# Kernel optimization log

Hardware: AMD Instinct MI355X
Metric: run time of the kernel (lower is better)

## Reference

```python
import jax, jax.numpy as jnp
import numpy as np
import math

B, C, IMG, P = 32, 3, 224, 16
E, DEPTH, H, MLP = 768, 12, 12, 3072
NP = (IMG // P) ** 2          # 196 patches
S = NP + 1                    # 197 tokens with cls
NCLS = 10
HD = E // H                   # 64 head dim
EPS = 1e-5


def setup_inputs() -> dict:
    key = jax.random.key(0)
    ks = iter(jax.random.split(key, 64))
    n = lambda shape, s=0.02: (jax.random.normal(next(ks), shape, jnp.float32) * s)
    inp = {
        "x": jax.random.normal(next(ks), (B, C, IMG, IMG), jnp.float32),
        "conv_w": n((E, C, P, P)),
        "conv_b": jnp.zeros((E,), jnp.float32),
        "cls_token": n((1, 1, E)),
        "pos_embed": n((1, S, E)),
        # stacked per-layer params, leading dim DEPTH; linear weights stored [in, out]
        "ln1_w": jnp.ones((DEPTH, E), jnp.float32),
        "ln1_b": jnp.zeros((DEPTH, E), jnp.float32),
        "qkv_w": n((DEPTH, E, 3 * E)),
        "qkv_b": jnp.zeros((DEPTH, 3 * E), jnp.float32),
        "proj_w": n((DEPTH, E, E)),
        "proj_b": jnp.zeros((DEPTH, E), jnp.float32),
        "ln2_w": jnp.ones((DEPTH, E), jnp.float32),
        "ln2_b": jnp.zeros((DEPTH, E), jnp.float32),
        "mlp_w1": n((DEPTH, E, MLP)),
        "mlp_b1": jnp.zeros((DEPTH, MLP), jnp.float32),
        "mlp_w2": n((DEPTH, MLP, E)),
        "mlp_b2": jnp.zeros((DEPTH, E), jnp.float32),
        "lnf_w": jnp.ones((E,), jnp.float32),
        "lnf_b": jnp.zeros((E,), jnp.float32),
        "head_w": n((E, NCLS)),
        "head_b": jnp.zeros((NCLS,), jnp.float32),
    }
    return inp


def layernorm(x, w, b):
    mu = jnp.mean(x, axis=-1, keepdims=True)
    var = jnp.mean(jnp.square(x - mu), axis=-1, keepdims=True)
    return (x - mu) * jax.lax.rsqrt(var + EPS) * w + b


def reference(x, conv_w, conv_b, cls_token, pos_embed,
              ln1_w, ln1_b, qkv_w, qkv_b, proj_w, proj_b,
              ln2_w, ln2_b, mlp_w1, mlp_b1, mlp_w2, mlp_b2,
              lnf_w, lnf_b, head_w, head_b):
    # --- patch embedding: stride-P, kernel-P conv == patchify + matmul ---
    g = IMG // P  # 14
    patches = x.reshape(B, C, g, P, g, P).transpose(0, 2, 4, 1, 3, 5).reshape(B, NP, C * P * P)
    wp = conv_w.reshape(E, C * P * P)
    tok = jnp.einsum('bpd,ed->bpe', patches, wp) + conv_b  # [B, NP, E]

    # cls token + positional embedding (dropout = identity at eval)
    h = jnp.concatenate([jnp.broadcast_to(cls_token, (B, 1, E)), tok], axis=1) + pos_embed

    scale = math.sqrt(HD)
    for i in range(DEPTH):
        # --- attention ---
        y = layernorm(h, ln1_w[i], ln1_b[i])
        qkv = (y @ qkv_w[i] + qkv_b[i]).reshape(B, S, 3, H, HD)
        q, k, v = qkv[:, :, 0], qkv[:, :, 1], qkv[:, :, 2]  # [B, S, H, HD]
        attn = jnp.einsum('bqhd,bkhd->bhqk', q, k) / scale
        attn = jax.nn.softmax(attn, axis=-1)
        o = jnp.einsum('bhqk,bkhd->bqhd', attn, v).reshape(B, S, E)
        h = h + (o @ proj_w[i] + proj_b[i])
        # --- MLP ---
        y = layernorm(h, ln2_w[i], ln2_b[i])
        y = jax.nn.gelu(y @ mlp_w1[i] + mlp_b1[i], approximate=False)
        h = h + (y @ mlp_w2[i] + mlp_b2[i])

    h = layernorm(h, lnf_w, lnf_b)
    return h[:, 0] @ head_w + head_b  # [B, NCLS]
```

## Files before the change

### kernel.cpp

```cpp
#include <hip/hip_runtime.h>


typedef __attribute__((ext_vector_type(8))) short short8;
typedef __attribute__((ext_vector_type(8))) unsigned short ushort8;
typedef __attribute__((ext_vector_type(4))) float f32x4;
typedef unsigned short u16;

#define DEV __device__ __forceinline__

DEV u16 f2bf(float f) {
  unsigned int u = __builtin_bit_cast(unsigned int, f);
  u += 0x7fffu + ((u >> 16) & 1u);
  return (u16)(u >> 16);
}
DEV float wred_sum(float v) {
  for (int o = 32; o; o >>= 1) v += __shfl_xor(v, o, 64);
  return v;
}
DEV void glds16(const void* gp, void* lp) {
  __builtin_amdgcn_global_load_lds(
      (const __attribute__((address_space(1))) void*)gp,
      (__attribute__((address_space(3))) void*)lp, 16, 0, 0);
}
DEV int xcd_swz(int flat, int nwg) {
  int q = nwg >> 3, r = nwg & 7;
  int x = flat & 7, o = flat >> 3;
  return (x < r ? x * (q + 1) : r * (q + 1) + (x - r) * q) + o;
}

__global__ __launch_bounds__(256) void cvt4_k(const float* __restrict__ s,
                                              u16* __restrict__ d, long n4) {
  long i = (long)blockIdx.x * 256 + threadIdx.x;
  if (i >= n4) return;
  float4 v = ((const float4*)s)[i];
  ushort4 o;
  o.x = f2bf(v.x); o.y = f2bf(v.y); o.z = f2bf(v.z); o.w = f2bf(v.w);
  ((ushort4*)d)[i] = o;
}

__global__ __launch_bounds__(256) void tpose_k(const float* __restrict__ s,
                                               u16* __restrict__ d, int K,
                                               int N) {
  __shared__ float t[32][33];
  const int bx = blockIdx.x;
  const int by = blockIdx.y;
  const size_t base = (size_t)blockIdx.z * K * N;
  const int c = threadIdx.x & 31, r0 = threadIdx.x >> 5;
#pragma unroll
  for (int i = 0; i < 4; ++i) {
    int r = r0 + i * 8;
    t[r][c] = s[base + (size_t)(by * 32 + r) * N + bx * 32 + c];
  }
  __syncthreads();
#pragma unroll
  for (int i = 0; i < 4; ++i) {
    int r = r0 + i * 8;
    d[base + (size_t)(bx * 32 + r) * K + by * 32 + c] = f2bf(t[c][r]);
  }
}

__global__ __launch_bounds__(256) void patch_k(const float* __restrict__ x,
                                               u16* __restrict__ pt) {
  int i = blockIdx.x * 256 + threadIdx.x;
  int d = i % 768;
  int bp = i / 768;
  int p = bp % 196, b = bp / 196;
  int c = d >> 8, pd = d & 255;
  int py = pd >> 4, px = pd & 15;
  int gy = p / 14, gx = p - gy * 14;
  size_t src = ((size_t)(b * 3 + c) * 224 + gy * 16 + py) * 224 + gx * 16 + px;
  pt[i] = f2bf(x[src]);
}

__global__ __launch_bounds__(256) void clspos_k(const float* __restrict__ cls,
                                                const float* __restrict__ pos,
                                                float* __restrict__ h) {
  int i = blockIdx.x * 256 + threadIdx.x;
  int b = i / 768, e = i - b * 768;
  h[(size_t)b * 197 * 768 + e] = cls[e] + pos[e];
}

template <int EPI, int BM>
__global__ __launch_bounds__(256) void gemmP(
    const u16* __restrict__ A, int lda, const u16* __restrict__ Bt, int ldb,
    const float* __restrict__ bias, u16* __restrict__ outb, int ldo,
    float* __restrict__ outf, const float* __restrict__ pos, int M, int N,
    int K) {
  constexpr int MI = BM / 32;
  __shared__ __align__(16) u16 Ak[2][BM * 32];
  __shared__ __align__(16) u16 Bk[2][128 * 32];
  const int tid = threadIdx.x;
  const int lane = tid & 63, wid = tid >> 6;
  const int wm = wid >> 1, wn = wid & 1;
  const int lg = lane >> 4, lr = lane & 15;
  const int nwg = gridDim.x * gridDim.y;
  const int wg = xcd_swz(blockIdx.y * gridDim.x + blockIdx.x, nwg);
  const int tn = wg % gridDim.x, tm = wg / gridDim.x;

  const int sr = lane >> 2;
  const int sc4 = (((lane & 3) ^ ((lane >> 3) & 3)) << 3);
  const u16* aSrc = A + (size_t)(tm * BM + wid * (BM / 4) + sr) * lda + sc4;
  const u16* bSrc = Bt + (size_t)(tn * 128 + wid * 32 + sr) * ldb + sc4;
  const size_t aRow16 = (size_t)16 * lda, bRow16 = (size_t)16 * ldb;

  auto stage = [&](int buf, int kt) {
    const u16* ak = aSrc + kt * 32;
    const u16* bk = bSrc + kt * 32;
    u16* ad = &Ak[buf][wid * (BM / 4) * 32];
    u16* bd = &Bk[buf][wid * 1024];
    glds16(ak, ad);
    if constexpr (BM == 128) glds16(ak + aRow16, ad + 512);
    glds16(bk, bd);
    glds16(bk + bRow16, bd + 512);
  };

  const int rp = (lg ^ ((lr >> 1) & 3)) << 3;
  f32x4 acc[MI][4] = {};
  auto compute = [&](int buf) {
    short8 af[MI], bfr[4];
#pragma unroll
    for (int i = 0; i < MI; ++i)
      af[i] =
          *(const short8*)(&Ak[buf][(wm * (BM / 2) + i * 16 + lr) * 32 + rp]);
#pragma unroll
    for (int i = 0; i < 4; ++i)
      bfr[i] = *(const short8*)(&Bk[buf][(wn * 64 + i * 16 + lr) * 32 + rp]);
#pragma unroll
    for (int mi = 0; mi < MI; ++mi)
#pragma unroll
      for (int ni = 0; ni < 4; ++ni)
        acc[mi][ni] = __builtin_amdgcn_mfma_f32_16x16x32_bf16(
            af[mi], bfr[ni], acc[mi][ni], 0, 0, 0);
  };

  const int nk = K >> 5;
  int cur = 0;
  stage(0, 0);
  __syncthreads();
  for (int kt = 0; kt < nk - 1; ++kt) {
    stage(cur ^ 1, kt + 1);
    compute(cur);
    __syncthreads();
    cur ^= 1;
  }
  compute(cur);

#pragma unroll
  for (int mi = 0; mi < MI; ++mi)
#pragma unroll
    for (int ni = 0; ni < 4; ++ni)
#pragma unroll
      for (int r = 0; r < 4; ++r) {
        int grow = tm * BM + wm * (BM / 2) + mi * 16 + lg * 4 + r;
        int gcol = tn * 128 + wn * 64 + ni * 16 + lr;
        if (grow < M) {
          float v = acc[mi][ni][r] + bias[gcol];
          if constexpr (EPI == 0) {
            outb[(size_t)grow * ldo + gcol] = f2bf(v);
          } else if constexpr (EPI == 1) {
            float u = __expf(-1.5957691216f * (v + 0.044715f * v * v * v));
            outb[(size_t)grow * ldo + gcol] = f2bf(v / (1.f + u));
          } else if constexpr (EPI == 2) {
            outf[(size_t)grow * ldo + gcol] += v;
          } else {
            int b = grow / 196, p = grow - b * 196;
            outf[(size_t)(grow + b + 1) * 768 + gcol] =
                v + pos[(size_t)(p + 1) * 768 + gcol];
          }
        }
      }
}

__global__ __launch_bounds__(64) void qksm_k(const u16* __restrict__ qkv,
                                             u16* __restrict__ P) {
  const int bh = blockIdx.x;
  const int qt = blockIdx.y;
  const int lane = threadIdx.x;
  const int lg = lane >> 4, lr = lane & 15;
  const int b = bh / 12, hh = bh - b * 12;
  const u16* base = qkv + (size_t)b * 197 * 2304 + hh * 64;
  int qrow = qt * 16 + lr;
  if (qrow > 196) qrow = 196;
  const u16* qp = base + (size_t)qrow * 2304 + lg * 8;
  short8 a0 = *(const short8*)(qp);
  short8 a1 = *(const short8*)(qp + 32);
  f32x4 c[13];
  const bool kval[2] = {true, (12 * 16 + lr) <= 196};
#pragma unroll
  for (int kt = 0; kt < 13; ++kt) {
    int krow = kt * 16 + lr;
    if (krow > 196) krow = 196;
    const u16* kp = base + 768 + (size_t)krow * 2304 + lg * 8;
    short8 b0 = *(const short8*)(kp);
    short8 b1 = *(const short8*)(kp + 32);
    f32x4 t = {0.f, 0.f, 0.f, 0.f};
    t = __builtin_amdgcn_mfma_f32_16x16x32_bf16(a0, b0, t, 0, 0, 0);
    c[kt] = __builtin_amdgcn_mfma_f32_16x16x32_bf16(a1, b1, t, 0, 0, 0);
  }
  float mr[4], sr_[4];
#pragma unroll
  for (int r = 0; r < 4; ++r) {
    float mm = -3.4e38f;
#pragma unroll
    for (int kt = 0; kt < 13; ++kt)
      if (kval[kt == 12]) mm = fmaxf(mm, c[kt][r] * 0.125f);
#pragma unroll
    for (int o = 1; o < 16; o <<= 1) mm = fmaxf(mm, __shfl_xor(mm, o, 64));
    mr[r] = mm;
  }
#pragma unroll
  for (int r = 0; r < 4; ++r) {
    float s = 0.f;
#pragma unroll
    for (int kt = 0; kt < 13; ++kt) {
      float e = kval[kt == 12] ? __expf(c[kt][r] * 0.125f - mr[r]) : 0.f;
      c[kt][r] = e;
      s += e;
    }
#pragma unroll
    for (int o = 1; o < 16; o <<= 1) s += __shfl_xor(s, o, 64);
    sr_[r] = 1.0f / s;
  }
  u16* pb = P + (size_t)bh * 197 * 224;
#pragma unroll
  for (int r = 0; r < 4; ++r) {
    int q = qt * 16 + lg * 4 + r;
    if (q < 197) {
#pragma unroll
      for (int kt = 0; kt < 13; ++kt)
        pb[(size_t)q * 224 + kt * 16 + lr] = f2bf(c[kt][r] * sr_[r]);
      pb[(size_t)q * 224 + 208 + lr] = 0;
    }
  }
}

__global__ __launch_bounds__(256) void pv_k(const u16* __restrict__ qkv,
                                            const u16* __restrict__ P,
                                            u16* __restrict__ o) {
  const int bh = blockIdx.x;
  const int b = bh / 12, hh = bh - b * 12;
  const int tid = threadIdx.x;
  const int lane = tid & 63, ct = tid >> 6;
  const int lg = lane >> 4, lr = lane & 15;
  const u16* vbase =
      qkv + (size_t)b * 197 * 2304 + 1536 + hh * 64 + ct * 16 + lr;
  short8 vf[7];
#pragma unroll
  for (int ks = 0; ks < 7; ++ks) {
    ushort8 t;
#pragma unroll
    for (int j = 0; j < 8; ++j) {
      int kk = ks * 32 + lg * 8 + j;
      if (kk > 196) kk = 196;
      t[j] = vbase[(size_t)kk * 2304];
    }
    vf[ks] = __builtin_bit_cast(short8, t);
  }
  const u16* pbase = P + (size_t)bh * 197 * 224;
  u16* ob = o + (size_t)b * 197 * 768 + hh * 64 + ct * 16;
  for (int qt = 0; qt < 13; ++qt) {
    int q = qt * 16 + lr;
    if (q > 196) q = 196;
    const u16* pp = pbase + (size_t)q * 224 + lg * 8;
    f32x4 acc = {0.f, 0.f, 0.f, 0.f};
#pragma unroll
    for (int ks = 0; ks < 7; ++ks) {
      short8 af = *(const short8*)(pp + ks * 32);
      acc = __builtin_amdgcn_mfma_f32_16x16x32_bf16(af, vf[ks], acc, 0, 0, 0);
    }
#pragma unroll
    for (int r = 0; r < 4; ++r) {
      int qq = qt * 16 + lg * 4 + r;
      if (qq < 197) ob[(size_t)qq * 768 + lr] = f2bf(acc[r]);
    }
  }
}

__global__ __launch_bounds__(256) void ln_k(const float* __restrict__ x,
                                            const float* __restrict__ w,
                                            const float* __restrict__ bb,
                                            u16* __restrict__ y) {
  const int r = blockIdx.x, tid = threadIdx.x;
  const float* xr = x + (size_t)r * 768;
  float v0 = xr[tid], v1 = xr[tid + 256], v2 = xr[tid + 512];
  float s = v0 + v1 + v2;
  float q = v0 * v0 + v1 * v1 + v2 * v2;
  s = wred_sum(s);
  q = wred_sum(q);
  __shared__ float ss[4], qs[4];
  int lane = tid & 63, wid = tid >> 6;
  if (lane == 0) { ss[wid] = s; qs[wid] = q; }
  __syncthreads();
  float S = ss[0] + ss[1] + ss[2] + ss[3];
  float Q = qs[0] + qs[1] + qs[2] + qs[3];
  float mu = S * (1.f / 768.f);
  float var = Q * (1.f / 768.f) - mu * mu;
  float rs = rsqrtf(var + 1e-5f);
  u16* yr = y + (size_t)r * 768;
  yr[tid] = f2bf((v0 - mu) * rs * w[tid] + bb[tid]);
  yr[tid + 256] = f2bf((v1 - mu) * rs * w[tid + 256] + bb[tid + 256]);
  yr[tid + 512] = f2bf((v2 - mu) * rs * w[tid + 512] + bb[tid + 512]);
}

__global__ __launch_bounds__(256) void head_k(
    const float* __restrict__ h, const float* __restrict__ lnw,
    const float* __restrict__ lnb, const float* __restrict__ hw,
    const float* __restrict__ hb, float* __restrict__ out) {
  const int b = blockIdx.x, tid = threadIdx.x;
  const float* xr = h + (size_t)b * 197 * 768;
  float v0 = xr[tid], v1 = xr[tid + 256], v2 = xr[tid + 512];
  float s = v0 + v1 + v2;
  float q = v0 * v0 + v1 * v1 + v2 * v2;
  s = wred_sum(s);
  q = wred_sum(q);
  __shared__ float ss[4], qs[4];
  int lane = tid & 63, wid = tid >> 6;
  if (lane == 0) { ss[wid] = s; qs[wid] = q; }
  __syncthreads();
  float S = ss[0] + ss[1] + ss[2] + ss[3];
  float Q = qs[0] + qs[1] + qs[2] + qs[3];
  float mu = S * (1.f / 768.f);
  float var = Q * (1.f / 768.f) - mu * mu;
  float rs = rsqrtf(var + 1e-5f);
  __shared__ float yb[768];
  yb[tid] = (v0 - mu) * rs * lnw[tid] + lnb[tid];
  yb[tid + 256] = (v1 - mu) * rs * lnw[tid + 256] + lnb[tid + 256];
  yb[tid + 512] = (v2 - mu) * rs * lnw[tid + 512] + lnb[tid + 512];
  __syncthreads();
  float p[10] = {};
  for (int e = tid; e < 768; e += 256) {
    float yv = yb[e];
#pragma unroll
    for (int n = 0; n < 10; ++n) p[n] += yv * hw[(size_t)e * 10 + n];
  }
#pragma unroll
  for (int n = 0; n < 10; ++n) p[n] = wred_sum(p[n]);
  __shared__ float red[4][10];
  if (lane == 0)
#pragma unroll
    for (int n = 0; n < 10; ++n) red[wid][n] = p[n];
  __syncthreads();
  if (tid < 10)
    out[b * 10 + tid] =
        red[0][tid] + red[1][tid] + red[2][tid] + red[3][tid] + hb[tid];
}

extern "C" void kernel_launch(void* const* d_in, const int* in_sizes, int n_in,
                              void* d_out, int out_size, void* d_ws,
                              size_t ws_size, hipStream_t stream) {
  const float* x = (const float*)d_in[0];
  const float* conv_w = (const float*)d_in[1];
  const float* conv_b = (const float*)d_in[2];
  const float* cls = (const float*)d_in[3];
  const float* pos = (const float*)d_in[4];
  const float* ln1w = (const float*)d_in[5];
  const float* ln1b = (const float*)d_in[6];
  const float* qkvw = (const float*)d_in[7];
  const float* qkvbias = (const float*)d_in[8];
  const float* projw = (const float*)d_in[9];
  const float* projb = (const float*)d_in[10];
  const float* ln2w = (const float*)d_in[11];
  const float* ln2b = (const float*)d_in[12];
  const float* w1f = (const float*)d_in[13];
  const float* b1 = (const float*)d_in[14];
  const float* w2f = (const float*)d_in[15];
  const float* b2 = (const float*)d_in[16];
  const float* lnfw = (const float*)d_in[17];
  const float* lnfb = (const float*)d_in[18];
  const float* headw = (const float*)d_in[19];
  const float* headb = (const float*)d_in[20];
  float* out = (float*)d_out;

  char* p = (char*)d_ws;
  auto take = [&](size_t bytes) {
    char* q = p;
    p += (bytes + 255) & ~(size_t)255;
    return q;
  };
  u16* wq = (u16*)take(12ull * 768 * 2304 * 2);
  u16* wpj = (u16*)take(12ull * 768 * 768 * 2);
  u16* w1 = (u16*)take(12ull * 768 * 3072 * 2);
  u16* w2 = (u16*)take(12ull * 3072 * 768 * 2);
  u16* wc = (u16*)take(768ull * 768 * 2);
  float* h = (float*)take(6304ull * 768 * 4);
  u16* y = (u16*)take(6400ull * 768 * 2);
  u16* qkv = (u16*)take(6400ull * 2304 * 2);
  u16* ob = (u16*)take(6400ull * 768 * 2);
  u16* mlpb = (u16*)take(6400ull * 3072 * 2);
  u16* P = (u16*)take(384ull * 197 * 224 * 2);
  (void)ws_size; (void)in_sizes; (void)n_in; (void)out_size;

  tpose_k<<<dim3(72, 24, 12), 256, 0, stream>>>(qkvw, wq, 768, 2304);
  tpose_k<<<dim3(24, 24, 12), 256, 0, stream>>>(projw, wpj, 768, 768);
  tpose_k<<<dim3(96, 24, 12), 256, 0, stream>>>(w1f, w1, 768, 3072);
  tpose_k<<<dim3(24, 96, 12), 256, 0, stream>>>(w2f, w2, 3072, 768);
  cvt4_k<<<576, 256, 0, stream>>>(conv_w, wc, 768 * 768 / 4);

  patch_k<<<6272 * 768 / 256, 256, 0, stream>>>(x, mlpb);
  gemmP<3, 64><<<dim3(6, 98), 256, 0, stream>>>(mlpb, 768, wc, 768, conv_b,
                                                nullptr, 0, h, pos, 6272, 768,
                                                768);
  clspos_k<<<32 * 768 / 256, 256, 0, stream>>>(cls, pos, h);

  for (int i = 0; i < 12; ++i) {
    ln_k<<<6304, 256, 0, stream>>>(h, ln1w + i * 768, ln1b + i * 768, y);
    gemmP<0, 128><<<dim3(18, 50), 256, 0, stream>>>(
        y, 768, wq + (size_t)i * 768 * 2304, 768, qkvbias + i * 2304, qkv,
        2304, nullptr, nullptr, 6304, 2304, 768);
    qksm_k<<<dim3(384, 13), 64, 0, stream>>>(qkv, P);
    pv_k<<<384, 256, 0, stream>>>(qkv, P, ob);
    gemmP<2, 64><<<dim3(6, 99), 256, 0, stream>>>(
        ob, 768, wpj + (size_t)i * 768 * 768, 768, projb + i * 768, nullptr,
        768, h, nullptr, 6304, 768, 768);
    ln_k<<<6304, 256, 0, stream>>>(h, ln2w + i * 768, ln2b + i * 768, y);
    gemmP<1, 128><<<dim3(24, 50), 256, 0, stream>>>(
        y, 768, w1 + (size_t)i * 768 * 3072, 768, b1 + i * 3072, mlpb, 3072,
        nullptr, nullptr, 6304, 3072, 768);
    gemmP<2, 64><<<dim3(6, 99), 256, 0, stream>>>(
        mlpb, 3072, w2 + (size_t)i * 3072 * 768, 3072, b2 + i * 768, nullptr,
        768, h, nullptr, 6304, 768, 3072);
  }

  head_k<<<32, 256, 0, stream>>>(h, lnfw, lnfb, headw, headb, out);
}
```

Measured before the change: 3.418 ms.

## Replace block-synchronized GEMM with per-wave private LDS tiles and no barriers

Every GEMM now runs with 2 waves per block, and each wave stages its own private copy of the 64-row A tile plus its own 64-column B slice into its own LDS region. This lets the k-loop drop __syncthreads and use only per-wave vmcnt waits. MFMA sections are also wrapped in s_setprio. In exchange, A tile loads are duplicated across the two waves, the tile is 64x128 for all GEMMs (QKV and MLP1 previously used 128-row tiles), and the vmcnt(8) count relies on each stage issuing exactly 8 loads.

```diff
diff --git a/kernel.cpp b/kernel.cpp
--- a/kernel.cpp
+++ b/kernel.cpp
@@ -80,18 +80,15 @@
   h[(size_t)b * 197 * 768 + e] = cls[e] + pos[e];
 }
 
-template <int EPI, int BM>
-__global__ __launch_bounds__(256) void gemmP(
+template <int EPI>
+__global__ __launch_bounds__(128) void gemmW(
     const u16* __restrict__ A, int lda, const u16* __restrict__ Bt, int ldb,
     const float* __restrict__ bias, u16* __restrict__ outb, int ldo,
     float* __restrict__ outf, const float* __restrict__ pos, int M, int N,
     int K) {
-  constexpr int MI = BM / 32;
-  __shared__ __align__(16) u16 Ak[2][BM * 32];
-  __shared__ __align__(16) u16 Bk[2][128 * 32];
+  __shared__ __align__(16) u16 Sm[2][2][2][2048];
   const int tid = threadIdx.x;
   const int lane = tid & 63, wid = tid >> 6;
-  const int wm = wid >> 1, wn = wid & 1;
   const int lg = lane >> 4, lr = lane & 15;
   const int nwg = gridDim.x * gridDim.y;
   const int wg = xcd_swz(blockIdx.y * gridDim.x + blockIdx.x, nwg);
@@ -99,60 +96,64 @@
 
   const int sr = lane >> 2;
   const int sc4 = (((lane & 3) ^ ((lane >> 3) & 3)) << 3);
-  const u16* aSrc = A + (size_t)(tm * BM + wid * (BM / 4) + sr) * lda + sc4;
-  const u16* bSrc = Bt + (size_t)(tn * 128 + wid * 32 + sr) * ldb + sc4;
-  const size_t aRow16 = (size_t)16 * lda, bRow16 = (size_t)16 * ldb;
+  const u16* aSrc = A + (size_t)(tm * 64 + sr) * lda + sc4;
+  const u16* bSrc = Bt + (size_t)(tn * 128 + wid * 64 + sr) * ldb + sc4;
 
   auto stage = [&](int buf, int kt) {
     const u16* ak = aSrc + kt * 32;
     const u16* bk = bSrc + kt * 32;
-    u16* ad = &Ak[buf][wid * (BM / 4) * 32];
-    u16* bd = &Bk[buf][wid * 1024];
-    glds16(ak, ad);
-    if constexpr (BM == 128) glds16(ak + aRow16, ad + 512);
-    glds16(bk, bd);
-    glds16(bk + bRow16, bd + 512);
+    u16* ad = &Sm[wid][buf][0][0];
+    u16* bd = &Sm[wid][buf][1][0];
+#pragma unroll
+    for (int c = 0; c < 4; ++c) {
+      glds16(ak + (size_t)(c * 16) * lda, ad + c * 512);
+      glds16(bk + (size_t)(c * 16) * ldb, bd + c * 512);
+    }
   };
 
   const int rp = (lg ^ ((lr >> 1) & 3)) << 3;
-  f32x4 acc[MI][4] = {};
+  f32x4 acc[4][4] = {};
   auto compute = [&](int buf) {
-    short8 af[MI], bfr[4];
-#pragma unroll
-    for (int i = 0; i < MI; ++i)
-      af[i] =
-          *(const short8*)(&Ak[buf][(wm * (BM / 2) + i * 16 + lr) * 32 + rp]);
-#pragma unroll
-    for (int i = 0; i < 4; ++i)
-      bfr[i] = *(const short8*)(&Bk[buf][(wn * 64 + i * 16 + lr) * 32 + rp]);
-#pragma unroll
-    for (int mi = 0; mi < MI; ++mi)
+    short8 af[4], bfr[4];
+    const u16* ab = &Sm[wid][buf][0][0];
+    const u16* bb = &Sm[wid][buf][1][0];
+#pragma unroll
+    for (int i = 0; i < 4; ++i) {
+      af[i] = *(const short8*)(ab + (i * 16 + lr) * 32 + rp);
+      bfr[i] = *(const short8*)(bb + (i * 16 + lr) * 32 + rp);
+    }
+    __builtin_amdgcn_s_setprio(1);
+#pragma unroll
+    for (int mi = 0; mi < 4; ++mi)
 #pragma unroll
       for (int ni = 0; ni < 4; ++ni)
         acc[mi][ni] = __builtin_amdgcn_mfma_f32_16x16x32_bf16(
             af[mi], bfr[ni], acc[mi][ni], 0, 0, 0);
+    __builtin_amdgcn_s_setprio(0);
   };
 
   const int nk = K >> 5;
   int cur = 0;
   stage(0, 0);
-  __syncthreads();
   for (int kt = 0; kt < nk - 1; ++kt) {
     stage(cur ^ 1, kt + 1);
+    asm volatile("s_waitcnt vmcnt(8)" ::: "memory");
+    __builtin_amdgcn_sched_barrier(0);
     compute(cur);
-    __syncthreads();
     cur ^= 1;
   }
+  asm volatile("s_waitcnt vmcnt(0)" ::: "memory");
+  __builtin_amdgcn_sched_barrier(0);
   compute(cur);
 
 #pragma unroll
-  for (int mi = 0; mi < MI; ++mi)
+  for (int mi = 0; mi < 4; ++mi)
 #pragma unroll
     for (int ni = 0; ni < 4; ++ni)
 #pragma unroll
       for (int r = 0; r < 4; ++r) {
-        int grow = tm * BM + wm * (BM / 2) + mi * 16 + lg * 4 + r;
-        int gcol = tn * 128 + wn * 64 + ni * 16 + lr;
+        int grow = tm * 64 + mi * 16 + lg * 4 + r;
+        int gcol = tn * 128 + wid * 64 + ni * 16 + lr;
         if (grow < M) {
           float v = acc[mi][ni][r] + bias[gcol];
           if constexpr (EPI == 0) {
@@ -397,26 +398,26 @@
   cvt4_k<<<576, 256, 0, stream>>>(conv_w, wc, 768 * 768 / 4);
 
   patch_k<<<6272 * 768 / 256, 256, 0, stream>>>(x, mlpb);
-  gemmP<3, 64><<<dim3(6, 98), 256, 0, stream>>>(mlpb, 768, wc, 768, conv_b,
-                                                nullptr, 0, h, pos, 6272, 768,
-                                                768);
+  gemmW<3><<<dim3(6, 98), 128, 0, stream>>>(mlpb, 768, wc, 768, conv_b,
+                                            nullptr, 0, h, pos, 6272, 768,
+                                            768);
   clspos_k<<<32 * 768 / 256, 256, 0, stream>>>(cls, pos, h);
 
   for (int i = 0; i < 12; ++i) {
     ln_k<<<6304, 256, 0, stream>>>(h, ln1w + i * 768, ln1b + i * 768, y);
-    gemmP<0, 128><<<dim3(18, 50), 256, 0, stream>>>(
+    gemmW<0><<<dim3(18, 99), 128, 0, stream>>>(
         y, 768, wq + (size_t)i * 768 * 2304, 768, qkvbias + i * 2304, qkv,
         2304, nullptr, nullptr, 6304, 2304, 768);
     qksm_k<<<dim3(384, 13), 64, 0, stream>>>(qkv, P);
     pv_k<<<384, 256, 0, stream>>>(qkv, P, ob);
-    gemmP<2, 64><<<dim3(6, 99), 256, 0, stream>>>(
+    gemmW<2><<<dim3(6, 99), 128, 0, stream>>>(
         ob, 768, wpj + (size_t)i * 768 * 768, 768, projb + i * 768, nullptr,
         768, h, nullptr, 6304, 768, 768);
     ln_k<<<6304, 256, 0, stream>>>(h, ln2w + i * 768, ln2b + i * 768, y);
-    gemmP<1, 128><<<dim3(24, 50), 256, 0, stream>>>(
+    gemmW<1><<<dim3(24, 99), 128, 0, stream>>>(
         y, 768, w1 + (size_t)i * 768 * 3072, 768, b1 + i * 3072, mlpb, 3072,
         nullptr, nullptr, 6304, 3072, 768);
-    gemmP<2, 64><<<dim3(6, 99), 256, 0, stream>>>(
+    gemmW<2><<<dim3(6, 99), 128, 0, stream>>>(
         mlpb, 3072, w2 + (size_t)i * 3072 * 768, 3072, b2 + i * 768, nullptr,
         768, h, nullptr, 6304, 768, 3072);
   }
```

Result: slower. 4.534 ms (+32.7%).

## Add 512-thread K64 GEMM kernel for QKV and MLP-up projections

Applied to the files above, without the earlier changes.

Introduces a new GEMM kernel using 8 waves per 128x128 tile with a K-step of 64 and XOR-swizzled LDS layout, and uses it for the QKV and first MLP GEMMs. Each wave computes a 64x32 sub-tile, halving the number of K iterations and barriers per tile and adding more waves per workgroup to hide latency. The epilogue is factored into a shared helper. The cost is larger LDS use (64 KB per block), which may limit occupancy, and fewer accumulators per wave.

```diff
diff --git a/kernel.cpp b/kernel.cpp
--- a/kernel.cpp
+++ b/kernel.cpp
@@ -78,6 +78,103 @@
   int i = blockIdx.x * 256 + threadIdx.x;
   int b = i / 768, e = i - b * 768;
   h[(size_t)b * 197 * 768 + e] = cls[e] + pos[e];
+}
+
+template <int EPI>
+DEV void epi_store(float v, int grow, int gcol, u16* outb, int ldo,
+                   float* outf, const float* pos) {
+  if constexpr (EPI == 0) {
+    outb[(size_t)grow * ldo + gcol] = f2bf(v);
+  } else if constexpr (EPI == 1) {
+    float u = __expf(-1.5957691216f * (v + 0.044715f * v * v * v));
+    outb[(size_t)grow * ldo + gcol] = f2bf(v / (1.f + u));
+  } else if constexpr (EPI == 2) {
+    outf[(size_t)grow * ldo + gcol] += v;
+  } else {
+    int b = grow / 196, p = grow - b * 196;
+    outf[(size_t)(grow + b + 1) * 768 + gcol] =
+        v + pos[(size_t)(p + 1) * 768 + gcol];
+  }
+}
+
+template <int EPI>
+__global__ __launch_bounds__(512) void gemmK64(
+    const u16* __restrict__ A, int lda, const u16* __restrict__ Bt, int ldb,
+    const float* __restrict__ bias, u16* __restrict__ outb, int ldo,
+    float* __restrict__ outf, const float* __restrict__ pos, int M, int N,
+    int K) {
+  __shared__ __align__(16) u16 Ak[2][128 * 64];
+  __shared__ __align__(16) u16 Bk[2][128 * 64];
+  const int tid = threadIdx.x;
+  const int lane = tid & 63, wid = tid >> 6;
+  const int wm = wid >> 2, wn = wid & 3;
+  const int lg = lane >> 4, lr = lane & 15;
+  const int nwg = gridDim.x * gridDim.y;
+  const int wg = xcd_swz(blockIdx.y * gridDim.x + blockIdx.x, nwg);
+  const int tn = wg % gridDim.x, tm = wg / gridDim.x;
+
+  const int r8 = lane >> 3, c8 = lane & 7;
+  const int swc = (c8 ^ r8) << 3;
+  const u16* aS = A + (size_t)(tm * 128 + wid * 16 + r8) * lda + swc;
+  const u16* bS = Bt + (size_t)(tn * 128 + wid * 16 + r8) * ldb + swc;
+
+  auto stage = [&](int buf, int kt) {
+    const u16* ak = aS + kt * 64;
+    const u16* bk = bS + kt * 64;
+    u16* ad = &Ak[buf][wid * 1024];
+    u16* bd = &Bk[buf][wid * 1024];
+    glds16(ak, ad);
+    glds16(ak + (size_t)8 * lda, ad + 512);
+    glds16(bk, bd);
+    glds16(bk + (size_t)8 * ldb, bd + 512);
+  };
+
+  f32x4 acc[4][2] = {};
+  auto compute = [&](int buf) {
+#pragma unroll
+    for (int ks = 0; ks < 2; ++ks) {
+      const int pc = (ks << 2) | lg;
+      const int po = ((pc ^ (lr & 7)) << 3);
+      short8 af[4], bf2[2];
+#pragma unroll
+      for (int i = 0; i < 4; ++i)
+        af[i] = *(const short8*)(&Ak[buf][(wm * 64 + i * 16 + lr) * 64 + po]);
+#pragma unroll
+      for (int i = 0; i < 2; ++i)
+        bf2[i] = *(const short8*)(&Bk[buf][(wn * 32 + i * 16 + lr) * 64 + po]);
+#pragma unroll
+      for (int mi = 0; mi < 4; ++mi)
+#pragma unroll
+        for (int ni = 0; ni < 2; ++ni)
+          acc[mi][ni] = __builtin_amdgcn_mfma_f32_16x16x32_bf16(
+              af[mi], bf2[ni], acc[mi][ni], 0, 0, 0);
+    }
+  };
+
+  const int nk = K >> 6;
+  int cur = 0;
+  stage(0, 0);
+  __syncthreads();
+  for (int kt = 0; kt < nk - 1; ++kt) {
+    stage(cur ^ 1, kt + 1);
+    compute(cur);
+    __syncthreads();
+    cur ^= 1;
+  }
+  compute(cur);
+
+#pragma unroll
+  for (int mi = 0; mi < 4; ++mi)
+#pragma unroll
+    for (int ni = 0; ni < 2; ++ni)
+#pragma unroll
+      for (int r = 0; r < 4; ++r) {
+        int grow = tm * 128 + wm * 64 + mi * 16 + lg * 4 + r;
+        int gcol = tn * 128 + wn * 32 + ni * 16 + lr;
+        if (grow < M)
+          epi_store<EPI>(acc[mi][ni][r] + bias[gcol], grow, gcol, outb, ldo,
+                         outf, pos);
+      }
 }
 
 template <int EPI, int BM>
@@ -153,21 +250,9 @@
       for (int r = 0; r < 4; ++r) {
         int grow = tm * BM + wm * (BM / 2) + mi * 16 + lg * 4 + r;
         int gcol = tn * 128 + wn * 64 + ni * 16 + lr;
-        if (grow < M) {
-          float v = acc[mi][ni][r] + bias[gcol];
-          if constexpr (EPI == 0) {
-            outb[(size_t)grow * ldo + gcol] = f2bf(v);
-          } else if constexpr (EPI == 1) {
-            float u = __expf(-1.5957691216f * (v + 0.044715f * v * v * v));
-            outb[(size_t)grow * ldo + gcol] = f2bf(v / (1.f + u));
-          } else if constexpr (EPI == 2) {
-            outf[(size_t)grow * ldo + gcol] += v;
-          } else {
-            int b = grow / 196, p = grow - b * 196;
-            outf[(size_t)(grow + b + 1) * 768 + gcol] =
-                v + pos[(size_t)(p + 1) * 768 + gcol];
-          }
-        }
+        if (grow < M)
+          epi_store<EPI>(acc[mi][ni][r] + bias[gcol], grow, gcol, outb, ldo,
+                         outf, pos);
       }
 }
 
@@ -404,7 +489,7 @@
 
   for (int i = 0; i < 12; ++i) {
     ln_k<<<6304, 256, 0, stream>>>(h, ln1w + i * 768, ln1b + i * 768, y);
-    gemmP<0, 128><<<dim3(18, 50), 256, 0, stream>>>(
+    gemmK64<0><<<dim3(18, 50), 512, 0, stream>>>(
         y, 768, wq + (size_t)i * 768 * 2304, 768, qkvbias + i * 2304, qkv,
         2304, nullptr, nullptr, 6304, 2304, 768);
     qksm_k<<<dim3(384, 13), 64, 0, stream>>>(qkv, P);
@@ -413,7 +498,7 @@
         ob, 768, wpj + (size_t)i * 768 * 768, 768, projb + i * 768, nullptr,
         768, h, nullptr, 6304, 768, 768);
     ln_k<<<6304, 256, 0, stream>>>(h, ln2w + i * 768, ln2b + i * 768, y);
-    gemmP<1, 128><<<dim3(24, 50), 256, 0, stream>>>(
+    gemmK64<1><<<dim3(24, 50), 512, 0, stream>>>(
         y, 768, w1 + (size_t)i * 768 * 3072, 768, b1 + i * 3072, mlpb, 3072,
         nullptr, nullptr, 6304, 3072, 768);
     gemmP<2, 64><<<dim3(6, 99), 256, 0, stream>>>(
```

After: 3.223 ms. 1.06x faster.
